# Kernel tuning notes

Measured on AMD Instinct MI355X. Metric: run time of the kernel, lower is better.

## Reference

```python
import jax, jax.numpy as jnp
import numpy as np

B, S, E = 2, 2048, 1024
H = 16
DK = E // H          # 64
ROT_DIM = 32         # min(32, embed_dim)
THETA = 10000.0


def _rope_tables(seq_len, dtype):
    # lucidrains RotaryEmbedding: inv_freq over even indices, repeated pairwise
    inv_freq = 1.0 / (THETA ** (jnp.arange(0, ROT_DIM, 2, dtype=jnp.float32) / ROT_DIM))
    t = jnp.arange(seq_len, dtype=jnp.float32)
    freqs = t[:, None] * inv_freq[None, :]            # [S, ROT_DIM/2]
    freqs = jnp.repeat(freqs, 2, axis=-1)             # [S, ROT_DIM] (interleaved repeat)
    return jnp.cos(freqs).astype(dtype), jnp.sin(freqs).astype(dtype)


def _rotate_half(x):
    # interleaved pairs: (x1, x2) -> (-x2, x1)
    x1 = x[..., 0::2]
    x2 = x[..., 1::2]
    return jnp.stack([-x2, x1], axis=-1).reshape(x.shape)


def _apply_rope(x, cos, sin):
    # x: [B, H, S, DK]; rotate first ROT_DIM dims, pass through the rest
    xr, xp = x[..., :ROT_DIM], x[..., ROT_DIM:]
    xr = xr * cos + _rotate_half(xr) * sin
    return jnp.concatenate([xr, xp], axis=-1)


def setup_inputs() -> dict:
    rng = jax.random.key(0)
    ks = jax.random.split(rng, 9)
    bound = 1.0 / np.sqrt(E)
    inp = {
        "query": jax.random.normal(ks[0], (B, S, E), dtype=jnp.float32),
        "key": jax.random.normal(ks[1], (B, S, E), dtype=jnp.float32),
        "value": jax.random.normal(ks[2], (B, S, E), dtype=jnp.float32),
        "Wq": jax.random.uniform(ks[3], (E, E), jnp.float32, -bound, bound),
        "bq": jax.random.uniform(ks[4], (E,), jnp.float32, -bound, bound),
        "Wk": jax.random.uniform(ks[5], (E, E), jnp.float32, -bound, bound),
        "bk": jax.random.uniform(ks[6], (E,), jnp.float32, -bound, bound),
        "Wv": jax.random.uniform(ks[7], (E, E), jnp.float32, -bound, bound),
        "bv": jax.random.uniform(ks[8], (E,), jnp.float32, -bound, bound),
    }
    return inp


def reference(query, key, value, Wq, bq, Wk, bk, Wv, bv):
    b, s, _ = query.shape
    # separate QKV linears (torch Linear: x @ W.T + b)
    q = query @ Wq.T + bq
    k = key @ Wk.T + bk
    v = value @ Wv.T + bv
    # [B, S, E] -> [B, H, S, DK]
    q = q.reshape(b, s, H, DK).transpose(0, 2, 1, 3)
    k = k.reshape(b, s, H, DK).transpose(0, 2, 1, 3)
    v = v.reshape(b, s, H, DK).transpose(0, 2, 1, 3)
    # rotary embedding on query and key
    cos, sin = _rope_tables(s, q.dtype)
    q = _apply_rope(q, cos, sin)
    k = _apply_rope(k, cos, sin)
    # scaled dot-product attention (no mask)
    scores = jnp.einsum('bhqd,bhkd->bhqk', q, k) / jnp.sqrt(jnp.asarray(DK, q.dtype))
    attn = jax.nn.softmax(scores, axis=-1)
    x = jnp.einsum('bhqk,bhkd->bhqd', attn, v)
    x = x.transpose(0, 2, 1, 3).reshape(b, s, H * DK)
    return (x, attn)
```

## Files before the change

### kernel.cpp

```cpp
#include <hip/hip_runtime.h>
#include <hip/hip_bf16.h>

#define B_  2
#define S_  2048
#define E_  1024
#define H_  16
#define DK_ 64
#define BH_ (B_*H_)
#define M_  (B_*S_)

typedef __attribute__((ext_vector_type(8))) short bf16x8;
typedef __attribute__((ext_vector_type(4))) float f32x4;
typedef unsigned short u16;
typedef unsigned int   u32;

__device__ __forceinline__ float bf2f(u16 u) {
    u32 x = ((u32)u) << 16;
    float f;
    __builtin_memcpy(&f, &x, 4);
    return f;
}
__device__ __forceinline__ u16 f2bf(float f) {
    u32 x;
    __builtin_memcpy(&x, &f, 4);
    u32 r = (x + 0x7fffu + ((x >> 16) & 1u)) >> 16;
    return (u16)r;
}

__device__ __forceinline__ void async16(const void* g, void* l) {
    __builtin_amdgcn_global_load_lds(
        (__attribute__((address_space(1))) void*)(g),
        (__attribute__((address_space(3))) void*)(l), 16, 0, 0);
}
__device__ __forceinline__ bf16x8 frag_at(const u16* base, int byteoff) {
    return *(const bf16x8*)((const char*)base + byteoff);
}

__device__ __forceinline__ void store8f(float* dst, const u16* src) {
    bf16x8 v = *(const bf16x8*)src;
    float4 lo = {bf2f((u16)v[0]), bf2f((u16)v[1]), bf2f((u16)v[2]), bf2f((u16)v[3])};
    float4 hi = {bf2f((u16)v[4]), bf2f((u16)v[5]), bf2f((u16)v[6]), bf2f((u16)v[7])};
    *(float4*)dst       = lo;
    *(float4*)(dst + 4) = hi;
}

__global__ void probe_kernel(const u16* __restrict__ w, int* __restrict__ flag)
{
    if (threadIdx.x == 0 && blockIdx.x == 0) {
        int big = 0;
        for (int i = 0; i < 128; i++) {
            float v = bf2f(w[i]);
            if (fabsf(v) > 0.25f) big++;
        }
        *flag = (big >= 4) ? 1 : 0;
    }
}

__global__ __launch_bounds__(256) void convert_kernel(
    const void* __restrict__ q, const void* __restrict__ k, const void* __restrict__ v,
    const void* __restrict__ wq, const void* __restrict__ wk, const void* __restrict__ wv,
    u16* __restrict__ dq, u16* __restrict__ dk, u16* __restrict__ dv,
    u16* __restrict__ ewq, u16* __restrict__ ewk, u16* __restrict__ ewv,
    const int* __restrict__ flag)
{
    const int y = blockIdx.y;
    const void* src; u16* dst; size_t n;
    switch (y) {
        case 0: src = q;  dst = dq;  n = (size_t)M_*E_; break;
        case 1: src = k;  dst = dk;  n = (size_t)M_*E_; break;
        case 2: src = v;  dst = dv;  n = (size_t)M_*E_; break;
        case 3: src = wq; dst = ewq; n = (size_t)E_*E_; break;
        case 4: src = wk; dst = ewk; n = (size_t)E_*E_; break;
        default:src = wv; dst = ewv; n = (size_t)E_*E_; break;
    }
    const size_t i = ((size_t)blockIdx.x * 256 + threadIdx.x) * 8;
    if (i >= n) return;
    if (*flag) {
        const float* s = (const float*)src + i;
        float4 f0 = *(const float4*)s;
        float4 f1 = *(const float4*)(s + 4);
        u16 tmp[8] = {f2bf(f0.x), f2bf(f0.y), f2bf(f0.z), f2bf(f0.w),
                      f2bf(f1.x), f2bf(f1.y), f2bf(f1.z), f2bf(f1.w)};
        *(uint4*)(dst + i) = *(uint4*)tmp;
    } else {
        *(uint4*)(dst + i) = *(const uint4*)((const u16*)src + i);
    }
}

__global__ __launch_bounds__(256) void proj_kernel(
    const u16* __restrict__ X, const u16* __restrict__ W,
    const void* __restrict__ biasv, u16* __restrict__ out, int vmode,
    const int* __restrict__ flag)
{
    __shared__ __align__(16) u16 als[128*64];
    __shared__ __align__(16) u16 bls[128*64];
    const int isf32 = *flag;
    const int t    = threadIdx.x;
    const int w    = t >> 6;
    const int ln   = t & 15;
    const int quad = (t >> 4) & 3;
    const int wr   = w >> 1;
    const int wc   = w & 1;
    const int m0   = blockIdx.x * 128;
    const int n0   = blockIdx.y * 128;
    const int l    = t & 63;
    const int srow = l >> 3;
    const int scsw = ((l & 7) * 16) ^ (srow << 4);
    const int rxor = (ln & 7) << 4;

    f32x4 acc[4][4];
    #pragma unroll
    for (int i = 0; i < 4; i++)
        #pragma unroll
        for (int j = 0; j < 4; j++) acc[i][j] = (f32x4){0.f, 0.f, 0.f, 0.f};

    for (int kt = 0; kt < E_; kt += 64) {
        __syncthreads();
        #pragma unroll
        for (int j = 0; j < 4; j++) {
            const int rowa = w*32 + j*8;
            async16(&X[(size_t)(m0 + rowa + srow)*E_ + kt + (scsw >> 1)], &als[rowa*64]);
            async16(&W[(size_t)(n0 + rowa + srow)*E_ + kt + (scsw >> 1)], &bls[rowa*64]);
        }
        __syncthreads();
        #pragma unroll
        for (int c = 0; c < 2; c++) {
            const int koff = c*64 + quad*16;
            bf16x8 a[4];
            #pragma unroll
            for (int mf = 0; mf < 4; mf++)
                a[mf] = frag_at(als, (wr*64 + mf*16 + ln)*128 + (koff ^ rxor));
            #pragma unroll
            for (int nf = 0; nf < 4; nf++) {
                bf16x8 b = frag_at(bls, (wc*64 + nf*16 + ln)*128 + (koff ^ rxor));
                #pragma unroll
                for (int mf = 0; mf < 4; mf++)
                    acc[mf][nf] = __builtin_amdgcn_mfma_f32_16x16x32_bf16(a[mf], b, acc[mf][nf], 0, 0, 0);
            }
        }
    }

    #pragma unroll
    for (int nf = 0; nf < 4; nf++) {
        const int n  = n0 + wc*64 + nf*16 + ln;
        const float bv = isf32 ? ((const float*)biasv)[n] : bf2f(((const u16*)biasv)[n]);
        const int h = n >> 6;
        const int d = n & 63;
        #pragma unroll
        for (int mf = 0; mf < 4; mf++) {
            #pragma unroll
            for (int r = 0; r < 4; r++) {
                const int m  = m0 + wr*64 + mf*16 + quad*4 + r;
                const int bb = m >> 11;
                const int s  = m & (S_ - 1);
                const float v = acc[mf][nf][r] + bv;
                size_t addr;
                if (vmode == 0) addr = (((size_t)(bb*H_ + h))*S_  + s)*DK_ + d;
                else            addr = (((size_t)(bb*H_ + h))*DK_ + d)*S_  + s;
                out[addr] = f2bf(v);
            }
        }
    }
}

__global__ __launch_bounds__(256) void rope_kernel(u16* __restrict__ qw, u16* __restrict__ kw)
{
    const int t   = threadIdx.x;
    const int pos = blockIdx.x * 8 + (t >> 5);
    const int j   = t & 31;
    const int isq = (blockIdx.y == 0);
    u16* base = (isq ? qw : kw) + (size_t)pos * DK_;
    const int s = pos & (S_ - 1);
    const float scale = isq ? 0.125f : 1.0f;
    if (j < 16) {
        const float invf = powf(10000.0f, -(float)(2*j) / 32.0f);
        const float ang  = (float)s * invf;
        float sn, cs;
        sincosf(ang, &sn, &cs);
        const float x0 = bf2f(base[2*j]);
        const float x1 = bf2f(base[2*j+1]);
        base[2*j]   = f2bf((x0*cs - x1*sn) * scale);
        base[2*j+1] = f2bf((x1*cs + x0*sn) * scale);
    } else if (isq) {
        const int d = j + 16;
        base[d]      = f2bf(bf2f(base[d])      * 0.125f);
        base[d+16]   = f2bf(bf2f(base[d+16])   * 0.125f);
    }
}

__global__ __launch_bounds__(256) void attn_kernel(
    const u16* __restrict__ qw, const u16* __restrict__ kw, const u16* __restrict__ vw,
    void* __restrict__ outbase, const int* __restrict__ flag)
{
    __shared__ __align__(16) u16 qls[64*72];
    __shared__ __align__(16) u16 pls[64*72];
    __shared__ __align__(16) u16 kls[64*64];
    __shared__ __align__(16) u16 vls[64*64];

    const int isf32 = *flag;
    const int t    = threadIdx.x;
    const int id   = blockIdx.y * gridDim.x + blockIdx.x;
    const int nid  = (id & 7) * 128 + (id >> 3);
    const int bh   = nid >> 5;
    const int q0   = (nid & 31) * 64;
    const int w    = t >> 6;
    const int ln   = t & 15;
    const int quad = (t >> 4) & 3;
    const int lr   = t >> 3;
    const int c8   = (t & 7) * 8;
    const int l    = t & 63;
    const int srow = l >> 3;
    const int scsw = ((l & 7) * 16) ^ (srow << 4);
    const int rxor = (ln & 7) << 4;

    const u16* qb = qw + (size_t)bh * S_ * DK_;
    const u16* kb = kw + (size_t)bh * S_ * DK_;
    const u16* vb = vw + (size_t)bh * DK_ * S_;

    *(uint4*)&qls[lr*72 + c8]      = *(const uint4*)&qb[(size_t)(q0+lr)*DK_    + c8];
    *(uint4*)&qls[(lr+32)*72 + c8] = *(const uint4*)&qb[(size_t)(q0+lr+32)*DK_ + c8];
    __syncthreads();
    bf16x8 qa[2];
    #pragma unroll
    for (int c = 0; c < 2; c++)
        qa[c] = *(const bf16x8*)&qls[(w*16+ln)*72 + c*32 + quad*8];

    float rs[4] = {0.f, 0.f, 0.f, 0.f};
    for (int kt = 0; kt < S_; kt += 64) {
        __syncthreads();
        #pragma unroll
        for (int j = 0; j < 2; j++) {
            const int rowa = w*16 + j*8;
            async16(&kb[(size_t)(kt + rowa + srow)*DK_ + (scsw >> 1)], &kls[rowa*64]);
        }
        __syncthreads();
        f32x4 sc[4];
        #pragma unroll
        for (int i = 0; i < 4; i++) sc[i] = (f32x4){0.f, 0.f, 0.f, 0.f};
        #pragma unroll
        for (int c = 0; c < 2; c++) {
            const int koff = c*64 + quad*16;
            #pragma unroll
            for (int cb = 0; cb < 4; cb++) {
                bf16x8 b = frag_at(kls, (cb*16+ln)*128 + (koff ^ rxor));
                sc[cb] = __builtin_amdgcn_mfma_f32_16x16x32_bf16(qa[c], b, sc[cb], 0, 0, 0);
            }
        }
        #pragma unroll
        for (int cb = 0; cb < 4; cb++)
            #pragma unroll
            for (int r = 0; r < 4; r++)
                rs[r] += expf(fminf(sc[cb][r], 60.0f));
    }
    #pragma unroll
    for (int r = 0; r < 4; r++) {
        rs[r] += __shfl_xor(rs[r], 1, 64);
        rs[r] += __shfl_xor(rs[r], 2, 64);
        rs[r] += __shfl_xor(rs[r], 4, 64);
        rs[r] += __shfl_xor(rs[r], 8, 64);
    }
    float inv[4];
    #pragma unroll
    for (int r = 0; r < 4; r++) inv[r] = 1.0f / rs[r];

    f32x4 xacc[4];
    #pragma unroll
    for (int i = 0; i < 4; i++) xacc[i] = (f32x4){0.f, 0.f, 0.f, 0.f};

    for (int kt = 0; kt < S_; kt += 64) {
        __syncthreads();
        #pragma unroll
        for (int j = 0; j < 2; j++) {
            const int rowa = w*16 + j*8;
            async16(&kb[(size_t)(kt + rowa + srow)*DK_ + (scsw >> 1)], &kls[rowa*64]);
            async16(&vb[(size_t)(rowa + srow)*S_ + kt + (scsw >> 1)],  &vls[rowa*64]);
        }
        __syncthreads();
        f32x4 sc[4];
        #pragma unroll
        for (int i = 0; i < 4; i++) sc[i] = (f32x4){0.f, 0.f, 0.f, 0.f};
        #pragma unroll
        for (int c = 0; c < 2; c++) {
            const int koff = c*64 + quad*16;
            #pragma unroll
            for (int cb = 0; cb < 4; cb++) {
                bf16x8 b = frag_at(kls, (cb*16+ln)*128 + (koff ^ rxor));
                sc[cb] = __builtin_amdgcn_mfma_f32_16x16x32_bf16(qa[c], b, sc[cb], 0, 0, 0);
            }
        }
        #pragma unroll
        for (int cb = 0; cb < 4; cb++)
            #pragma unroll
            for (int r = 0; r < 4; r++) {
                const float p = expf(fminf(sc[cb][r], 60.0f)) * inv[r];
                pls[(w*16 + quad*4 + r)*72 + cb*16 + ln] = f2bf(p);
            }
        __syncthreads();
        {
            const size_t a0 = ((size_t)bh*S_ + (q0+lr))*S_ + kt + c8;
            const size_t a1 = ((size_t)bh*S_ + (q0+lr+32))*S_ + kt + c8;
            if (isf32) {
                float* af = (float*)outbase + (size_t)M_*E_;
                store8f(&af[a0], &pls[lr*72 + c8]);
                store8f(&af[a1], &pls[(lr+32)*72 + c8]);
            } else {
                u16* au = (u16*)outbase + (size_t)M_*E_;
                *(uint4*)&au[a0] = *(const uint4*)&pls[lr*72 + c8];
                *(uint4*)&au[a1] = *(const uint4*)&pls[(lr+32)*72 + c8];
            }
        }
        #pragma unroll
        for (int c = 0; c < 2; c++) {
            const int koff = c*64 + quad*16;
            bf16x8 pa = *(const bf16x8*)&pls[(w*16+ln)*72 + c*32 + quad*8];
            #pragma unroll
            for (int cb = 0; cb < 4; cb++) {
                bf16x8 b = frag_at(vls, (cb*16+ln)*128 + (koff ^ rxor));
                xacc[cb] = __builtin_amdgcn_mfma_f32_16x16x32_bf16(pa, b, xacc[cb], 0, 0, 0);
            }
        }
    }

    const int bb = bh >> 4;
    const int h  = bh & 15;
    #pragma unroll
    for (int cb = 0; cb < 4; cb++) {
        const int d = cb*16 + ln;
        #pragma unroll
        for (int r = 0; r < 4; r++) {
            const int s = q0 + w*16 + quad*4 + r;
            const size_t idx = (((size_t)bb*S_ + s)*H_ + h)*DK_ + d;
            if (isf32) ((float*)outbase)[idx] = xacc[cb][r];
            else       ((u16*)outbase)[idx]   = f2bf(xacc[cb][r]);
        }
    }
}

extern "C" void kernel_launch(void* const* d_in, const int* in_sizes, int n_in,
                              void* d_out, int out_size, void* d_ws, size_t ws_size,
                              hipStream_t stream)
{
    const void* query = d_in[0];
    const void* key   = d_in[1];
    const void* value = d_in[2];
    const void* Wq    = d_in[3];
    const void* bq    = d_in[4];
    const void* Wk    = d_in[5];
    const void* bk    = d_in[6];
    const void* Wv    = d_in[7];
    const void* bv    = d_in[8];

    int* flag = (int*)d_ws;
    u16* qws  = (u16*)((char*)d_ws + 64);
    u16* kws  = qws + (size_t)M_ * E_;
    u16* vws  = kws + (size_t)M_ * E_;
    u16* xq   = vws + (size_t)M_ * E_;
    u16* xk   = xq  + (size_t)M_ * E_;
    u16* xv   = xk  + (size_t)M_ * E_;
    u16* wqc  = xv  + (size_t)M_ * E_;
    u16* wkc  = wqc + (size_t)E_ * E_;
    u16* wvc  = wkc + (size_t)E_ * E_;

    probe_kernel<<<1, 64, 0, stream>>>((const u16*)Wq, flag);
    convert_kernel<<<dim3(2048, 6), 256, 0, stream>>>(
        query, key, value, Wq, Wk, Wv, xq, xk, xv, wqc, wkc, wvc, flag);

    dim3 gp(M_/128, E_/128);
    proj_kernel<<<gp, 256, 0, stream>>>(xq, wqc, bq, qws, 0, flag);
    proj_kernel<<<gp, 256, 0, stream>>>(xk, wkc, bk, kws, 0, flag);
    proj_kernel<<<gp, 256, 0, stream>>>(xv, wvc, bv, vws, 1, flag);
    rope_kernel<<<dim3(BH_*S_/8, 2), 256, 0, stream>>>(qws, kws);
    attn_kernel<<<dim3(S_/64, BH_), 256, 0, stream>>>(qws, kws, vws, d_out, flag);
}
```

Measured before the change: 868.2 us.

## Fuse RoPE into batched QKV projection and double attention query tile

The three projection launches become one launch with grid z selecting Q, K or V, and the RoPE rotation plus the query scaling move into the projection epilogue using a lane shuffle to fetch the paired element. This removes the separate rope kernel and its extra read-modify-write pass over Q and K. The attention kernel now processes 128 query rows per block (two 16-row MFMA fragments per wave), so each K/V tile loaded into shared memory is reused twice as much and the grid is halved. In exchange, register pressure and LDS use per block go up, and the epilogue now computes sincos per element.

After: 812.1 us. 1.07x faster.

```diff
diff --git a/kernel.cpp b/kernel.cpp
--- a/kernel.cpp
+++ b/kernel.cpp
@@ -88,13 +88,21 @@
 }
 
 __global__ __launch_bounds__(256) void proj_kernel(
-    const u16* __restrict__ X, const u16* __restrict__ W,
-    const void* __restrict__ biasv, u16* __restrict__ out, int vmode,
+    const u16* __restrict__ Xq, const u16* __restrict__ Xk, const u16* __restrict__ Xv,
+    const u16* __restrict__ Wqp, const u16* __restrict__ Wkp, const u16* __restrict__ Wvp,
+    const void* __restrict__ bqv, const void* __restrict__ bkv, const void* __restrict__ bvv,
+    u16* __restrict__ qo, u16* __restrict__ ko, u16* __restrict__ vo,
     const int* __restrict__ flag)
 {
     __shared__ __align__(16) u16 als[128*64];
     __shared__ __align__(16) u16 bls[128*64];
     const int isf32 = *flag;
+    const int z = blockIdx.z;
+    const u16* X = (z==0) ? Xq  : ((z==1) ? Xk  : Xv);
+    const u16* W = (z==0) ? Wqp : ((z==1) ? Wkp : Wvp);
+    const void* biasv = (z==0) ? bqv : ((z==1) ? bkv : bvv);
+    u16* out = (z==0) ? qo : ((z==1) ? ko : vo);
+
     const int t    = threadIdx.x;
     const int w    = t >> 6;
     const int ln   = t & 15;
@@ -140,12 +148,17 @@
         }
     }
 
+    const float scale = (z == 0) ? 0.125f : 1.0f;
     #pragma unroll
     for (int nf = 0; nf < 4; nf++) {
         const int n  = n0 + wc*64 + nf*16 + ln;
-        const float bv = isf32 ? ((const float*)biasv)[n] : bf2f(((const u16*)biasv)[n]);
+        const float bvf = isf32 ? ((const float*)biasv)[n] : bf2f(((const u16*)biasv)[n]);
         const int h = n >> 6;
         const int d = n & 63;
+        const int dorope = (z <= 1) && (d < 32);
+        const float sgn  = (d & 1) ? 1.0f : -1.0f;
+        float invf = 0.f;
+        if (dorope) invf = powf(10000.0f, -(float)(d & ~1) / 32.0f);
         #pragma unroll
         for (int mf = 0; mf < 4; mf++) {
             #pragma unroll
@@ -153,38 +166,20 @@
                 const int m  = m0 + wr*64 + mf*16 + quad*4 + r;
                 const int bb = m >> 11;
                 const int s  = m & (S_ - 1);
-                const float v = acc[mf][nf][r] + bv;
+                float v = acc[mf][nf][r] + bvf;
+                if (dorope) {
+                    const float vp = __shfl_xor(v, 1, 64);
+                    float sn, cs;
+                    sincosf((float)s * invf, &sn, &cs);
+                    v = v*cs + sgn*vp*sn;
+                }
+                v *= scale;
                 size_t addr;
-                if (vmode == 0) addr = (((size_t)(bb*H_ + h))*S_  + s)*DK_ + d;
-                else            addr = (((size_t)(bb*H_ + h))*DK_ + d)*S_  + s;
+                if (z == 2) addr = (((size_t)(bb*H_ + h))*DK_ + d)*S_  + s;
+                else        addr = (((size_t)(bb*H_ + h))*S_  + s)*DK_ + d;
                 out[addr] = f2bf(v);
             }
         }
-    }
-}
-
-__global__ __launch_bounds__(256) void rope_kernel(u16* __restrict__ qw, u16* __restrict__ kw)
-{
-    const int t   = threadIdx.x;
-    const int pos = blockIdx.x * 8 + (t >> 5);
-    const int j   = t & 31;
-    const int isq = (blockIdx.y == 0);
-    u16* base = (isq ? qw : kw) + (size_t)pos * DK_;
-    const int s = pos & (S_ - 1);
-    const float scale = isq ? 0.125f : 1.0f;
-    if (j < 16) {
-        const float invf = powf(10000.0f, -(float)(2*j) / 32.0f);
-        const float ang  = (float)s * invf;
-        float sn, cs;
-        sincosf(ang, &sn, &cs);
-        const float x0 = bf2f(base[2*j]);
-        const float x1 = bf2f(base[2*j+1]);
-        base[2*j]   = f2bf((x0*cs - x1*sn) * scale);
-        base[2*j+1] = f2bf((x1*cs + x0*sn) * scale);
-    } else if (isq) {
-        const int d = j + 16;
-        base[d]      = f2bf(bf2f(base[d])      * 0.125f);
-        base[d+16]   = f2bf(bf2f(base[d+16])   * 0.125f);
     }
 }
 
@@ -192,17 +187,16 @@
     const u16* __restrict__ qw, const u16* __restrict__ kw, const u16* __restrict__ vw,
     void* __restrict__ outbase, const int* __restrict__ flag)
 {
-    __shared__ __align__(16) u16 qls[64*72];
-    __shared__ __align__(16) u16 pls[64*72];
-    __shared__ __align__(16) u16 kls[64*64];
+    __shared__ __align__(16) u16 sstage[128*64];
     __shared__ __align__(16) u16 vls[64*64];
+    __shared__ __align__(16) u16 pls[128*72];
 
     const int isf32 = *flag;
     const int t    = threadIdx.x;
     const int id   = blockIdx.y * gridDim.x + blockIdx.x;
-    const int nid  = (id & 7) * 128 + (id >> 3);
-    const int bh   = nid >> 5;
-    const int q0   = (nid & 31) * 64;
+    const int nid  = (id & 7) * 64 + (id >> 3);
+    const int bh   = nid >> 4;
+    const int q0   = (nid & 15) * 128;
     const int w    = t >> 6;
     const int ln   = t & 15;
     const int quad = (t >> 4) & 3;
@@ -217,106 +211,131 @@
     const u16* kb = kw + (size_t)bh * S_ * DK_;
     const u16* vb = vw + (size_t)bh * DK_ * S_;
 
-    *(uint4*)&qls[lr*72 + c8]      = *(const uint4*)&qb[(size_t)(q0+lr)*DK_    + c8];
-    *(uint4*)&qls[(lr+32)*72 + c8] = *(const uint4*)&qb[(size_t)(q0+lr+32)*DK_ + c8];
+    #pragma unroll
+    for (int j = 0; j < 4; j++) {
+        const int rowa = w*32 + j*8;
+        async16(&qb[(size_t)(q0 + rowa + srow)*DK_ + (scsw >> 1)], &sstage[rowa*64]);
+    }
     __syncthreads();
-    bf16x8 qa[2];
-    #pragma unroll
-    for (int c = 0; c < 2; c++)
-        qa[c] = *(const bf16x8*)&qls[(w*16+ln)*72 + c*32 + quad*8];
-
-    float rs[4] = {0.f, 0.f, 0.f, 0.f};
+    bf16x8 qa[2][2];
+    #pragma unroll
+    for (int m = 0; m < 2; m++)
+        #pragma unroll
+        for (int c = 0; c < 2; c++)
+            qa[m][c] = frag_at(sstage, (w*32 + m*16 + ln)*128 + ((c*64 + quad*16) ^ rxor));
+
+    float rs[2][4];
+    #pragma unroll
+    for (int m = 0; m < 2; m++)
+        #pragma unroll
+        for (int r = 0; r < 4; r++) rs[m][r] = 0.f;
+
     for (int kt = 0; kt < S_; kt += 64) {
         __syncthreads();
         #pragma unroll
         for (int j = 0; j < 2; j++) {
             const int rowa = w*16 + j*8;
-            async16(&kb[(size_t)(kt + rowa + srow)*DK_ + (scsw >> 1)], &kls[rowa*64]);
-        }
-        __syncthreads();
-        f32x4 sc[4];
-        #pragma unroll
-        for (int i = 0; i < 4; i++) sc[i] = (f32x4){0.f, 0.f, 0.f, 0.f};
+            async16(&kb[(size_t)(kt + rowa + srow)*DK_ + (scsw >> 1)], &sstage[rowa*64]);
+        }
+        __syncthreads();
+        f32x4 sc[2][4];
+        #pragma unroll
+        for (int m = 0; m < 2; m++)
+            #pragma unroll
+            for (int cb = 0; cb < 4; cb++) sc[m][cb] = (f32x4){0.f, 0.f, 0.f, 0.f};
         #pragma unroll
         for (int c = 0; c < 2; c++) {
             const int koff = c*64 + quad*16;
             #pragma unroll
             for (int cb = 0; cb < 4; cb++) {
-                bf16x8 b = frag_at(kls, (cb*16+ln)*128 + (koff ^ rxor));
-                sc[cb] = __builtin_amdgcn_mfma_f32_16x16x32_bf16(qa[c], b, sc[cb], 0, 0, 0);
-            }
-        }
-        #pragma unroll
-        for (int cb = 0; cb < 4; cb++)
-            #pragma unroll
-            for (int r = 0; r < 4; r++)
-                rs[r] += expf(fminf(sc[cb][r], 60.0f));
-    }
-    #pragma unroll
-    for (int r = 0; r < 4; r++) {
-        rs[r] += __shfl_xor(rs[r], 1, 64);
-        rs[r] += __shfl_xor(rs[r], 2, 64);
-        rs[r] += __shfl_xor(rs[r], 4, 64);
-        rs[r] += __shfl_xor(rs[r], 8, 64);
-    }
-    float inv[4];
-    #pragma unroll
-    for (int r = 0; r < 4; r++) inv[r] = 1.0f / rs[r];
-
-    f32x4 xacc[4];
-    #pragma unroll
-    for (int i = 0; i < 4; i++) xacc[i] = (f32x4){0.f, 0.f, 0.f, 0.f};
+                bf16x8 b = frag_at(sstage, (cb*16+ln)*128 + (koff ^ rxor));
+                #pragma unroll
+                for (int m = 0; m < 2; m++)
+                    sc[m][cb] = __builtin_amdgcn_mfma_f32_16x16x32_bf16(qa[m][c], b, sc[m][cb], 0, 0, 0);
+            }
+        }
+        #pragma unroll
+        for (int m = 0; m < 2; m++)
+            #pragma unroll
+            for (int cb = 0; cb < 4; cb++)
+                #pragma unroll
+                for (int r = 0; r < 4; r++)
+                    rs[m][r] += expf(fminf(sc[m][cb][r], 60.0f));
+    }
+    float inv[2][4];
+    #pragma unroll
+    for (int m = 0; m < 2; m++)
+        #pragma unroll
+        for (int r = 0; r < 4; r++) {
+            float x = rs[m][r];
+            x += __shfl_xor(x, 1, 64);
+            x += __shfl_xor(x, 2, 64);
+            x += __shfl_xor(x, 4, 64);
+            x += __shfl_xor(x, 8, 64);
+            inv[m][r] = 1.0f / x;
+        }
+
+    f32x4 xacc[2][4];
+    #pragma unroll
+    for (int m = 0; m < 2; m++)
+        #pragma unroll
+        for (int cb = 0; cb < 4; cb++) xacc[m][cb] = (f32x4){0.f, 0.f, 0.f, 0.f};
 
     for (int kt = 0; kt < S_; kt += 64) {
         __syncthreads();
         #pragma unroll
         for (int j = 0; j < 2; j++) {
             const int rowa = w*16 + j*8;
-            async16(&kb[(size_t)(kt + rowa + srow)*DK_ + (scsw >> 1)], &kls[rowa*64]);
+            async16(&kb[(size_t)(kt + rowa + srow)*DK_ + (scsw >> 1)], &sstage[rowa*64]);
             async16(&vb[(size_t)(rowa + srow)*S_ + kt + (scsw >> 1)],  &vls[rowa*64]);
         }
         __syncthreads();
-        f32x4 sc[4];
-        #pragma unroll
-        for (int i = 0; i < 4; i++) sc[i] = (f32x4){0.f, 0.f, 0.f, 0.f};
+        f32x4 sc[2][4];
+        #pragma unroll
+        for (int m = 0; m < 2; m++)
+            #pragma unroll
+            for (int cb = 0; cb < 4; cb++) sc[m][cb] = (f32x4){0.f, 0.f, 0.f, 0.f};
         #pragma unroll
         for (int c = 0; c < 2; c++) {
             const int koff = c*64 + quad*16;
             #pragma unroll
             for (int cb = 0; cb < 4; cb++) {
-                bf16x8 b = frag_at(kls, (cb*16+ln)*128 + (koff ^ rxor));
-                sc[cb] = __builtin_amdgcn_mfma_f32_16x16x32_bf16(qa[c], b, sc[cb], 0, 0, 0);
-            }
-        }
-        #pragma unroll
-        for (int cb = 0; cb < 4; cb++)
-            #pragma unroll
-            for (int r = 0; r < 4; r++) {
-                const float p = expf(fminf(sc[cb][r], 60.0f)) * inv[r];
-                pls[(w*16 + quad*4 + r)*72 + cb*16 + ln] = f2bf(p);
-            }
-        __syncthreads();
-        {
-            const size_t a0 = ((size_t)bh*S_ + (q0+lr))*S_ + kt + c8;
-            const size_t a1 = ((size_t)bh*S_ + (q0+lr+32))*S_ + kt + c8;
-            if (isf32) {
-                float* af = (float*)outbase + (size_t)M_*E_;
-                store8f(&af[a0], &pls[lr*72 + c8]);
-                store8f(&af[a1], &pls[(lr+32)*72 + c8]);
-            } else {
-                u16* au = (u16*)outbase + (size_t)M_*E_;
-                *(uint4*)&au[a0] = *(const uint4*)&pls[lr*72 + c8];
-                *(uint4*)&au[a1] = *(const uint4*)&pls[(lr+32)*72 + c8];
-            }
+                bf16x8 b = frag_at(sstage, (cb*16+ln)*128 + (koff ^ rxor));
+                #pragma unroll
+                for (int m = 0; m < 2; m++)
+                    sc[m][cb] = __builtin_amdgcn_mfma_f32_16x16x32_bf16(qa[m][c], b, sc[m][cb], 0, 0, 0);
+            }
+        }
+        #pragma unroll
+        for (int m = 0; m < 2; m++)
+            #pragma unroll
+            for (int cb = 0; cb < 4; cb++)
+                #pragma unroll
+                for (int r = 0; r < 4; r++) {
+                    const float p = expf(fminf(sc[m][cb][r], 60.0f)) * inv[m][r];
+                    pls[(w*32 + m*16 + quad*4 + r)*72 + cb*16 + ln] = f2bf(p);
+                }
+        __syncthreads();
+        #pragma unroll
+        for (int rep = 0; rep < 4; rep++) {
+            const int row = lr + rep*32;
+            const size_t a = ((size_t)bh*S_ + (q0 + row))*S_ + kt + c8;
+            if (isf32) store8f((float*)outbase + (size_t)M_*E_ + a, &pls[row*72 + c8]);
+            else       *(uint4*)((u16*)outbase + (size_t)M_*E_ + a) = *(const uint4*)&pls[row*72 + c8];
         }
         #pragma unroll
         for (int c = 0; c < 2; c++) {
             const int koff = c*64 + quad*16;
-            bf16x8 pa = *(const bf16x8*)&pls[(w*16+ln)*72 + c*32 + quad*8];
+            bf16x8 pa[2];
+            #pragma unroll
+            for (int m = 0; m < 2; m++)
+                pa[m] = *(const bf16x8*)&pls[(w*32 + m*16 + ln)*72 + c*32 + quad*8];
             #pragma unroll
             for (int cb = 0; cb < 4; cb++) {
                 bf16x8 b = frag_at(vls, (cb*16+ln)*128 + (koff ^ rxor));
-                xacc[cb] = __builtin_amdgcn_mfma_f32_16x16x32_bf16(pa, b, xacc[cb], 0, 0, 0);
+                #pragma unroll
+                for (int m = 0; m < 2; m++)
+                    xacc[m][cb] = __builtin_amdgcn_mfma_f32_16x16x32_bf16(pa[m], b, xacc[m][cb], 0, 0, 0);
             }
         }
     }
@@ -324,16 +343,18 @@
     const int bb = bh >> 4;
     const int h  = bh & 15;
     #pragma unroll
-    for (int cb = 0; cb < 4; cb++) {
-        const int d = cb*16 + ln;
-        #pragma unroll
-        for (int r = 0; r < 4; r++) {
-            const int s = q0 + w*16 + quad*4 + r;
-            const size_t idx = (((size_t)bb*S_ + s)*H_ + h)*DK_ + d;
-            if (isf32) ((float*)outbase)[idx] = xacc[cb][r];
-            else       ((u16*)outbase)[idx]   = f2bf(xacc[cb][r]);
-        }
-    }
+    for (int m = 0; m < 2; m++)
+        #pragma unroll
+        for (int cb = 0; cb < 4; cb++) {
+            const int d = cb*16 + ln;
+            #pragma unroll
+            for (int r = 0; r < 4; r++) {
+                const int s = q0 + w*32 + m*16 + quad*4 + r;
+                const size_t idx = (((size_t)bb*S_ + s)*H_ + h)*DK_ + d;
+                if (isf32) ((float*)outbase)[idx] = xacc[m][cb][r];
+                else       ((u16*)outbase)[idx]   = f2bf(xacc[m][cb][r]);
+            }
+        }
 }
 
 extern "C" void kernel_launch(void* const* d_in, const int* in_sizes, int n_in,
@@ -365,10 +386,8 @@
     convert_kernel<<<dim3(2048, 6), 256, 0, stream>>>(
         query, key, value, Wq, Wk, Wv, xq, xk, xv, wqc, wkc, wvc, flag);
 
-    dim3 gp(M_/128, E_/128);
-    proj_kernel<<<gp, 256, 0, stream>>>(xq, wqc, bq, qws, 0, flag);
-    proj_kernel<<<gp, 256, 0, stream>>>(xk, wkc, bk, kws, 0, flag);
-    proj_kernel<<<gp, 256, 0, stream>>>(xv, wvc, bv, vws, 1, flag);
-    rope_kernel<<<dim3(BH_*S_/8, 2), 256, 0, stream>>>(qws, kws);
-    attn_kernel<<<dim3(S_/64, BH_), 256, 0, stream>>>(qws, kws, vws, d_out, flag);
-}
+    proj_kernel<<<dim3(M_/128, E_/128, 3), 256, 0, stream>>>(
+        xq, xk, xv, wqc, wkc, wvc, bq, bk, bv, qws, kws, vws, flag);
+
+    attn_kernel<<<dim3(S_/128, BH_), 256, 0, stream>>>(qws, kws, vws, d_out, flag);
+}
```
